# Kernel optimization log

Measured on AMD Instinct MI355X. Metric: run time of the kernel, lower is better.

## Reference

```python
import jax, jax.numpy as jnp
import numpy as np

N = 20000      # nodes
E = 320000     # edges (avg degree 16)
D_IN = 128     # input_dim
HID = 128      # graph_hidden_dim (per-head channels)
HEADS = 4


def setup_inputs() -> dict:
    key = jax.random.key(0)
    ks = jax.random.split(key, 16)
    def gl(k, shape, fan_in):
        return jax.random.normal(k, shape, jnp.float32) / np.float32(np.sqrt(fan_in))
    x = jax.random.normal(ks[0], (N, D_IN), jnp.float32)
    edge_index = jax.random.randint(ks[1], (2, E), 0, N, dtype=jnp.int64)
    # layer 0: in=D_IN, heads=4, concat -> 4*HID
    W0 = gl(ks[2], (D_IN, HEADS * HID), D_IN)
    a_src0 = gl(ks[3], (HEADS, HID), HID)
    a_dst0 = gl(ks[4], (HEADS, HID), HID)
    b0 = jnp.zeros((HEADS * HID,), jnp.float32)
    # layer 1: in=4*HID, heads=4, concat -> 4*HID
    W1 = gl(ks[5], (HEADS * HID, HEADS * HID), HEADS * HID)
    a_src1 = gl(ks[6], (HEADS, HID), HID)
    a_dst1 = gl(ks[7], (HEADS, HID), HID)
    b1 = jnp.zeros((HEADS * HID,), jnp.float32)
    # layer 2: in=4*HID, heads=1, no concat -> HID
    W2 = gl(ks[8], (HEADS * HID, HID), HEADS * HID)
    a_src2 = gl(ks[9], (1, HID), HID)
    a_dst2 = gl(ks[10], (1, HID), HID)
    b2 = jnp.zeros((HID,), jnp.float32)
    # output MLP: HID -> HID//2 -> 1
    Wm1 = gl(ks[11], (HID, HID // 2), HID)
    bm1 = jnp.zeros((HID // 2,), jnp.float32)
    Wm2 = gl(ks[12], (HID // 2, 1), HID // 2)
    bm2 = jnp.zeros((1,), jnp.float32)
    return dict(x=x, edge_index=edge_index, W0=W0, a_src0=a_src0, a_dst0=a_dst0, b0=b0,
                W1=W1, a_src1=a_src1, a_dst1=a_dst1, b1=b1,
                W2=W2, a_src2=a_src2, a_dst2=a_dst2, b2=b2,
                Wm1=Wm1, bm1=bm1, Wm2=Wm2, bm2=bm2)


def _gat(x, src, dst, W, a_s, a_d, b, heads, ch, concat):
    """PyG GATConv: per-head linear, edge attention with LeakyReLU(0.2),
    segment softmax over incoming edges, scatter-add aggregation."""
    n = x.shape[0]
    xl = (x @ W).reshape(n, heads, ch)                      # [N,H,C]
    a_src_n = jnp.einsum('nhc,hc->nh', xl, a_s)             # [N,H]
    a_dst_n = jnp.einsum('nhc,hc->nh', xl, a_d)
    e = jax.nn.leaky_relu(a_src_n[src] + a_dst_n[dst], 0.2) # [E,H]
    m = jax.ops.segment_max(e, dst, num_segments=n)
    ex = jnp.exp(e - m[dst])
    den = jax.ops.segment_sum(ex, dst, num_segments=n)
    alpha = ex / den[dst]                                   # self-loops keep den > 0
    out = jax.ops.segment_sum(alpha[:, :, None] * xl[src], dst, num_segments=n)  # [N,H,C]
    out = out.reshape(n, heads * ch) if concat else out.mean(axis=1)
    return out + b


def reference(x, edge_index, W0, a_src0, a_dst0, b0, W1, a_src1, a_dst1, b1,
              W2, a_src2, a_dst2, b2, Wm1, bm1, Wm2, bm2):
    n = x.shape[0]
    loops = jnp.arange(n, dtype=edge_index.dtype)           # add_self_loops (PyG default)
    src = jnp.concatenate([edge_index[0], loops])
    dst = jnp.concatenate([edge_index[1], loops])
    h = jax.nn.relu(_gat(x, src, dst, W0, a_src0, a_dst0, b0, HEADS, HID, True))
    h = jax.nn.relu(_gat(h, src, dst, W1, a_src1, a_dst1, b1, HEADS, HID, True))
    h = _gat(h, src, dst, W2, a_src2, a_dst2, b2, 1, HID, False)
    g = h.mean(axis=0, keepdims=True)                       # global mean pool, batch=None -> [1,HID]
    g = jax.nn.relu(g @ Wm1 + bm1)
    return g @ Wm2 + bm2                                    # predictions [1,1]
```

## Files before the change

### kernel.cpp

```cpp
#include <hip/hip_runtime.h>
#include <math.h>


#define MAXDEG 96

typedef float f32x4 __attribute__((ext_vector_type(4)));
typedef float f32x2 __attribute__((ext_vector_type(2)));
typedef short s16x8 __attribute__((ext_vector_type(8)));
typedef short s16x4 __attribute__((ext_vector_type(4)));

__device__ inline ushort f2bf(float f) {
  unsigned u = __float_as_uint(f);
  u += 0x7FFF + ((u >> 16) & 1);
  return (ushort)(u >> 16);
}
__device__ inline float bf2f(ushort h) { return __uint_as_float((unsigned)h << 16); }
__device__ inline unsigned char f2fp8(float f) {
  int p = __builtin_amdgcn_cvt_pk_fp8_f32(f, f, 0, false);
  return (unsigned char)(p & 0xFF);
}

__global__ void prep_kernel(
    const float* __restrict__ W0, const float* __restrict__ W1,
    const float* __restrict__ W2, ushort* __restrict__ w0h, ushort* __restrict__ w0l,
    ushort* __restrict__ w1h, ushort* __restrict__ w1l, ushort* __restrict__ w2h,
    ushort* __restrict__ w2l, int* __restrict__ zero_region, int zcount) {
  int idx = blockIdx.x * 256 + threadIdx.x;
  if (idx < zcount) zero_region[idx] = 0;
  const float* W; ushort *th, *tl; int K, N;
  if (idx < 16384)      { W = W0; th = w0h; tl = w0l; K = 128; N = 512; }
  else if (idx < 81920) { idx -= 16384; W = W1; th = w1h; tl = w1l; K = 512; N = 512; }
  else                  { idx -= 81920; W = W2; th = w2h; tl = w2l; K = 512; N = 128; }
  int nn = idx % N;
  int k4 = (idx / N) << 2;
  s16x4 hv, lv;
#pragma unroll
  for (int r = 0; r < 4; ++r) {
    float w = W[(size_t)(k4 + r) * N + nn];
    ushort h = f2bf(w);
    hv[r] = (short)h;
    lv[r] = (short)f2bf(w - bf2f(h));
  }
  *(s16x4*)&th[(size_t)nn * K + k4] = hv;
  *(s16x4*)&tl[(size_t)nn * K + k4] = lv;
}

template <int NC>
__device__ inline void gemm_epilogue(
    f32x4 (&acc)[2][4], unsigned char* __restrict__ Cb, const float* __restrict__ a_s,
    const float* __restrict__ a_d, float* __restrict__ asn, float* __restrict__ adn,
    float (*st_sh)[64][2], int M, int row0, int col0, int hidx,
    int tid, int lane, int wid, int wm, int wn, int fr) {
  constexpr int N = NC * 128;
  float asv[4], adv[4];
#pragma unroll
  for (int j = 0; j < 4; ++j) {
    asv[j] = a_s[hidx * 128 + wn + j * 16 + fr];
    adv[j] = a_d[hidx * 128 + wn + j * 16 + fr];
  }
  int rb = row0 + wm + ((lane >> 4) << 2);
  int cb = col0 + wn + fr;
#pragma unroll
  for (int i = 0; i < 2; ++i)
#pragma unroll
    for (int r = 0; r < 4; ++r) {
      int row = rb + i * 16 + r;
      float sp = 0.f, dp = 0.f;
#pragma unroll
      for (int j = 0; j < 4; ++j) {
        float c = acc[i][j][r];
        sp += c * asv[j];
        dp += c * adv[j];
        if (row < M) Cb[(size_t)row * N + cb + j * 16] = f2fp8(c);
      }
#pragma unroll
      for (int m = 1; m < 16; m <<= 1) {
        sp += __shfl_xor(sp, m);
        dp += __shfl_xor(dp, m);
      }
      if ((lane & 15) == 0) {
        int rowb = wm + i * 16 + ((lane >> 4) << 2) + r;
        st_sh[0][rowb][wid >> 1] = sp;
        st_sh[1][rowb][wid >> 1] = dp;
      }
    }
  __syncthreads();
  if (tid < 64) {
    int row = row0 + tid;
    if (row < M) {
      asn[(size_t)row * NC + hidx] = st_sh[0][tid][0] + st_sh[0][tid][1];
      adn[(size_t)row * NC + hidx] = st_sh[1][tid][0] + st_sh[1][tid][1];
    }
  }
}

template <int NC>
__global__ __launch_bounds__(256, 2) void gemm0_scatter_kernel(
    const float* __restrict__ A, const ushort* __restrict__ Bth,
    const ushort* __restrict__ Btl, unsigned char* __restrict__ Cb,
    const float* __restrict__ a_s, const float* __restrict__ a_d,
    float* __restrict__ asn, float* __restrict__ adn,
    int M, int K,
    const int* __restrict__ ei, int* __restrict__ cursor, int* __restrict__ srcs,
    int E, int n, int scb) {
  __shared__ s16x8 Ash[4][64], Asl[4][64];
  __shared__ s16x8 Bsh[4][128], Bsl[4][128];
  __shared__ float st_sh[2][64][2];

  if ((int)blockIdx.x < scb) {
    int t = blockIdx.x * 256 + threadIdx.x;
    int s, d;
    if (t < E)          { s = ei[t]; d = ei[E + t]; }
    else if (t < E + n) { s = t - E; d = s; }
    else return;
    int pos = atomicAdd(&cursor[d], 1);
    if (pos < MAXDEG) srcs[d * MAXDEG + pos] = s;
    return;
  }

  int id = blockIdx.x - scb;
  int rs = (id / (8 * NC)) * 8 + (id & 7);
  int row0 = rs * 64;
  if (row0 >= M) return;
  int hidx = (id >> 3) % NC;
  int col0 = hidx * 128;
  int tid = threadIdx.x;
  int am = tid >> 2, aq = tid & 3;
  int bn = tid >> 1, bq = (tid & 1) << 1;
  int lane = tid & 63, wid = tid >> 6;
  int wm = (wid & 1) << 5, wn = (wid >> 1) << 6;
  int fr = lane & 15, fqq = lane >> 4;
  f32x4 acc[2][4] = {};
  const float* Arow = A + (size_t)(row0 + am) * K + aq * 8;
  bool avalid = (row0 + am) < M;
  const ushort* bhp = Bth + (size_t)(col0 + bn) * K + bq * 8;
  const ushort* blp = Btl + (size_t)(col0 + bn) * K + bq * 8;

  for (int k0 = 0; k0 < K; k0 += 32) {
    float v[8];
    if (avalid) {
      float4 t0 = *(const float4*)(Arow + k0);
      float4 t1 = *(const float4*)(Arow + k0 + 4);
      v[0] = t0.x; v[1] = t0.y; v[2] = t0.z; v[3] = t0.w;
      v[4] = t1.x; v[5] = t1.y; v[6] = t1.z; v[7] = t1.w;
    } else {
#pragma unroll
      for (int r = 0; r < 8; ++r) v[r] = 0.f;
    }
    s16x8 hv, lv;
#pragma unroll
    for (int r = 0; r < 8; ++r) {
      ushort h = f2bf(v[r]);
      hv[r] = (short)h;
      lv[r] = (short)f2bf(v[r] - bf2f(h));
    }
    Ash[aq][am] = hv;
    Asl[aq][am] = lv;
    Bsh[bq][bn]     = *(const s16x8*)(bhp + k0);
    Bsh[bq + 1][bn] = *(const s16x8*)(bhp + k0 + 8);
    Bsl[bq][bn]     = *(const s16x8*)(blp + k0);
    Bsl[bq + 1][bn] = *(const s16x8*)(blp + k0 + 8);
    __syncthreads();
    s16x8 ah[2], al[2], bh[4], bl[4];
#pragma unroll
    for (int i = 0; i < 2; ++i) {
      ah[i] = Ash[fqq][wm + i * 16 + fr];
      al[i] = Asl[fqq][wm + i * 16 + fr];
    }
#pragma unroll
    for (int j = 0; j < 4; ++j) {
      bh[j] = Bsh[fqq][wn + j * 16 + fr];
      bl[j] = Bsl[fqq][wn + j * 16 + fr];
    }
#pragma unroll
    for (int i = 0; i < 2; ++i)
#pragma unroll
      for (int j = 0; j < 4; ++j) {
        acc[i][j] = __builtin_amdgcn_mfma_f32_16x16x32_bf16(ah[i], bh[j], acc[i][j], 0, 0, 0);
        acc[i][j] = __builtin_amdgcn_mfma_f32_16x16x32_bf16(ah[i], bl[j], acc[i][j], 0, 0, 0);
        acc[i][j] = __builtin_amdgcn_mfma_f32_16x16x32_bf16(al[i], bh[j], acc[i][j], 0, 0, 0);
      }
    __syncthreads();
  }
  gemm_epilogue<NC>(acc, Cb, a_s, a_d, asn, adn, st_sh, M, row0, col0, hidx,
                    tid, lane, wid, wm, wn, fr);
}

template <int NC>
__global__ __launch_bounds__(256, 2) void gemm_bf16a_kernel(
    const ushort* __restrict__ A, const ushort* __restrict__ Bth,
    const ushort* __restrict__ Btl, unsigned char* __restrict__ Cb,
    const float* __restrict__ a_s, const float* __restrict__ a_d,
    float* __restrict__ asn, float* __restrict__ adn,
    int M, int K) {
  __shared__ s16x8 Ash[4][64];
  __shared__ s16x8 Bsh[4][128], Bsl[4][128];
  __shared__ float st_sh[2][64][2];
  int id = blockIdx.x;
  int rs = (id / (8 * NC)) * 8 + (id & 7);
  int row0 = rs * 64;
  if (row0 >= M) return;
  int hidx = (id >> 3) % NC;
  int col0 = hidx * 128;
  int tid = threadIdx.x;
  int am = tid >> 2, aq = tid & 3;
  int bn = tid >> 1, bq = (tid & 1) << 1;
  int lane = tid & 63, wid = tid >> 6;
  int wm = (wid & 1) << 5, wn = (wid >> 1) << 6;
  int fr = lane & 15, fqq = lane >> 4;
  f32x4 acc[2][4] = {};
  const ushort* Arow = A + (size_t)(row0 + am) * K + aq * 8;
  bool avalid = (row0 + am) < M;
  const ushort* bhp = Bth + (size_t)(col0 + bn) * K + bq * 8;
  const ushort* blp = Btl + (size_t)(col0 + bn) * K + bq * 8;
  const s16x8 zero8 = {};

  for (int k0 = 0; k0 < K; k0 += 32) {
    Ash[aq][am] = avalid ? *(const s16x8*)(Arow + k0) : zero8;
    Bsh[bq][bn]     = *(const s16x8*)(bhp + k0);
    Bsh[bq + 1][bn] = *(const s16x8*)(bhp + k0 + 8);
    Bsl[bq][bn]     = *(const s16x8*)(blp + k0);
    Bsl[bq + 1][bn] = *(const s16x8*)(blp + k0 + 8);
    __syncthreads();
    s16x8 ah[2], bh[4], bl[4];
#pragma unroll
    for (int i = 0; i < 2; ++i) ah[i] = Ash[fqq][wm + i * 16 + fr];
#pragma unroll
    for (int j = 0; j < 4; ++j) {
      bh[j] = Bsh[fqq][wn + j * 16 + fr];
      bl[j] = Bsl[fqq][wn + j * 16 + fr];
    }
#pragma unroll
    for (int i = 0; i < 2; ++i)
#pragma unroll
      for (int j = 0; j < 4; ++j) {
        acc[i][j] = __builtin_amdgcn_mfma_f32_16x16x32_bf16(ah[i], bh[j], acc[i][j], 0, 0, 0);
        acc[i][j] = __builtin_amdgcn_mfma_f32_16x16x32_bf16(ah[i], bl[j], acc[i][j], 0, 0, 0);
      }
    __syncthreads();
  }
  gemm_epilogue<NC>(acc, Cb, a_s, a_d, asn, adn, st_sh, M, row0, col0, hidx,
                    tid, lane, wid, wm, wn, fr);
}

template <int NC>
__global__ __launch_bounds__(256, 2) void gemm_bf16a128_kernel(
    const ushort* __restrict__ A, const ushort* __restrict__ Bth,
    const ushort* __restrict__ Btl, unsigned char* __restrict__ Cb,
    const float* __restrict__ a_s, const float* __restrict__ a_d,
    float* __restrict__ asn, float* __restrict__ adn,
    int M, int K) {
  constexpr int N = NC * 128;
  __shared__ s16x8 Ash[4][128];
  __shared__ s16x8 Bsh[4][128], Bsl[4][128];
  __shared__ float st_sh[2][128][2];
  int id = blockIdx.x;
  int rs = (id / (8 * NC)) * 8 + (id & 7);
  int row0 = rs * 128;
  if (row0 >= M) return;
  int hidx = (id >> 3) % NC;
  int col0 = hidx * 128;
  int tid = threadIdx.x;
  int am = tid >> 1, aq = (tid & 1) << 1;
  int bn = tid >> 1, bq = (tid & 1) << 1;
  int lane = tid & 63, wid = tid >> 6;
  int wm = (wid & 1) << 6, wn = (wid >> 1) << 6;
  int fr = lane & 15, fqq = lane >> 4;
  f32x4 acc[4][4] = {};
  const ushort* Arow = A + (size_t)(row0 + am) * K + aq * 8;
  bool avalid = (row0 + am) < M;
  const ushort* bhp = Bth + (size_t)(col0 + bn) * K + bq * 8;
  const ushort* blp = Btl + (size_t)(col0 + bn) * K + bq * 8;
  const s16x8 zero8 = {};

  for (int k0 = 0; k0 < K; k0 += 32) {
    Ash[aq][am]     = avalid ? *(const s16x8*)(Arow + k0) : zero8;
    Ash[aq + 1][am] = avalid ? *(const s16x8*)(Arow + k0 + 8) : zero8;
    Bsh[bq][bn]     = *(const s16x8*)(bhp + k0);
    Bsh[bq + 1][bn] = *(const s16x8*)(bhp + k0 + 8);
    Bsl[bq][bn]     = *(const s16x8*)(blp + k0);
    Bsl[bq + 1][bn] = *(const s16x8*)(blp + k0 + 8);
    __syncthreads();
    s16x8 ah[4], bh[4], bl[4];
#pragma unroll
    for (int i = 0; i < 4; ++i) ah[i] = Ash[fqq][wm + i * 16 + fr];
#pragma unroll
    for (int j = 0; j < 4; ++j) {
      bh[j] = Bsh[fqq][wn + j * 16 + fr];
      bl[j] = Bsl[fqq][wn + j * 16 + fr];
    }
#pragma unroll
    for (int i = 0; i < 4; ++i)
#pragma unroll
      for (int j = 0; j < 4; ++j) {
        acc[i][j] = __builtin_amdgcn_mfma_f32_16x16x32_bf16(ah[i], bh[j], acc[i][j], 0, 0, 0);
        acc[i][j] = __builtin_amdgcn_mfma_f32_16x16x32_bf16(ah[i], bl[j], acc[i][j], 0, 0, 0);
      }
    __syncthreads();
  }
  float asv[4], adv[4];
#pragma unroll
  for (int j = 0; j < 4; ++j) {
    asv[j] = a_s[hidx * 128 + wn + j * 16 + fr];
    adv[j] = a_d[hidx * 128 + wn + j * 16 + fr];
  }
  int rb = row0 + wm + ((lane >> 4) << 2);
  int cb = col0 + wn + fr;
#pragma unroll
  for (int i = 0; i < 4; ++i)
#pragma unroll
    for (int r = 0; r < 4; ++r) {
      int row = rb + i * 16 + r;
      float sp = 0.f, dp = 0.f;
#pragma unroll
      for (int j = 0; j < 4; ++j) {
        float c = acc[i][j][r];
        sp += c * asv[j];
        dp += c * adv[j];
        if (row < M) Cb[(size_t)row * N + cb + j * 16] = f2fp8(c);
      }
#pragma unroll
      for (int m = 1; m < 16; m <<= 1) {
        sp += __shfl_xor(sp, m);
        dp += __shfl_xor(dp, m);
      }
      if ((lane & 15) == 0) {
        int rowb = wm + i * 16 + ((lane >> 4) << 2) + r;
        st_sh[0][rowb][wid >> 1] = sp;
        st_sh[1][rowb][wid >> 1] = dp;
      }
    }
  __syncthreads();
  if (tid < 128) {
    int row = row0 + tid;
    if (row < M) {
      asn[(size_t)row * NC + hidx] = st_sh[0][tid][0] + st_sh[0][tid][1];
      adn[(size_t)row * NC + hidx] = st_sh[1][tid][0] + st_sh[1][tid][1];
    }
  }
}

__global__ __launch_bounds__(256) void agg4_kernel(
    const unsigned char* __restrict__ xl, const float* __restrict__ asn,
    const float* __restrict__ adn, const int* __restrict__ srcs,
    const int* __restrict__ degs, const float* __restrict__ bias,
    ushort* __restrict__ out, int n) {
  __shared__ float alpha_sh[4][4][64];
  __shared__ int src_sh[4][64];
  int wib = threadIdx.x >> 6, lane = threadIdx.x & 63;
  int nd = blockIdx.x * 4 + wib;
  if (nd >= n) return;
  int beg = nd * MAXDEG;
  int deg = min(degs[nd], MAXDEG);
  float4 adl = *(const float4*)&adn[(size_t)nd * 4];
  int ch0 = lane << 3;
  int hm = lane >> 4;
  float den[4] = {0.f, 0.f, 0.f, 0.f};
  float acc[8] = {};

  for (int j0 = 0; j0 < deg; j0 += 64) {
    int j = j0 + lane;
    int s = 0;
    float w0 = 0.f, w1 = 0.f, w2 = 0.f, w3 = 0.f;
    if (j < deg) {
      s = srcs[beg + j];
      float4 av = *(const float4*)&asn[(size_t)s * 4];
      float e;
      e = av.x + adl.x; e = (e > 0.f) ? e : 0.2f * e; w0 = __expf(fminf(e, 30.f));
      e = av.y + adl.y; e = (e > 0.f) ? e : 0.2f * e; w1 = __expf(fminf(e, 30.f));
      e = av.z + adl.z; e = (e > 0.f) ? e : 0.2f * e; w2 = __expf(fminf(e, 30.f));
      e = av.w + adl.w; e = (e > 0.f) ? e : 0.2f * e; w3 = __expf(fminf(e, 30.f));
      den[0] += w0; den[1] += w1; den[2] += w2; den[3] += w3;
    }
    src_sh[wib][lane] = s;
    alpha_sh[wib][0][lane] = w0;
    alpha_sh[wib][1][lane] = w1;
    alpha_sh[wib][2][lane] = w2;
    alpha_sh[wib][3][lane] = w3;
    __builtin_amdgcn_wave_barrier();
    int cl = min(64, deg - j0);
    int jj = 0;
    for (; jj + 8 <= cl; jj += 8) {
      int4 sv0 = *(const int4*)&src_sh[wib][jj];
      int4 sv1 = *(const int4*)&src_sh[wib][jj + 4];
      float4 av0 = *(const float4*)&alpha_sh[wib][hm][jj];
      float4 av1 = *(const float4*)&alpha_sh[wib][hm][jj + 4];
      uint2 v[8];
      v[0] = *(const uint2*)(xl + (size_t)sv0.x * 512 + ch0);
      v[1] = *(const uint2*)(xl + (size_t)sv0.y * 512 + ch0);
      v[2] = *(const uint2*)(xl + (size_t)sv0.z * 512 + ch0);
      v[3] = *(const uint2*)(xl + (size_t)sv0.w * 512 + ch0);
      v[4] = *(const uint2*)(xl + (size_t)sv1.x * 512 + ch0);
      v[5] = *(const uint2*)(xl + (size_t)sv1.y * 512 + ch0);
      v[6] = *(const uint2*)(xl + (size_t)sv1.z * 512 + ch0);
      v[7] = *(const uint2*)(xl + (size_t)sv1.w * 512 + ch0);
      float a[8] = {av0.x, av0.y, av0.z, av0.w, av1.x, av1.y, av1.z, av1.w};
#pragma unroll
      for (int u = 0; u < 8; ++u) {
        f32x2 c01 = __builtin_amdgcn_cvt_pk_f32_fp8((int)v[u].x, false);
        f32x2 c23 = __builtin_amdgcn_cvt_pk_f32_fp8((int)v[u].x, true);
        f32x2 c45 = __builtin_amdgcn_cvt_pk_f32_fp8((int)v[u].y, false);
        f32x2 c67 = __builtin_amdgcn_cvt_pk_f32_fp8((int)v[u].y, true);
        acc[0] += a[u] * c01[0]; acc[1] += a[u] * c01[1];
        acc[2] += a[u] * c23[0]; acc[3] += a[u] * c23[1];
        acc[4] += a[u] * c45[0]; acc[5] += a[u] * c45[1];
        acc[6] += a[u] * c67[0]; acc[7] += a[u] * c67[1];
      }
    }
    for (; jj < cl; ++jj) {
      int s2 = src_sh[wib][jj];
      float a = alpha_sh[wib][hm][jj];
      uint2 v = *(const uint2*)(xl + (size_t)s2 * 512 + ch0);
      f32x2 c01 = __builtin_amdgcn_cvt_pk_f32_fp8((int)v.x, false);
      f32x2 c23 = __builtin_amdgcn_cvt_pk_f32_fp8((int)v.x, true);
      f32x2 c45 = __builtin_amdgcn_cvt_pk_f32_fp8((int)v.y, false);
      f32x2 c67 = __builtin_amdgcn_cvt_pk_f32_fp8((int)v.y, true);
      acc[0] += a * c01[0]; acc[1] += a * c01[1];
      acc[2] += a * c23[0]; acc[3] += a * c23[1];
      acc[4] += a * c45[0]; acc[5] += a * c45[1];
      acc[6] += a * c67[0]; acc[7] += a * c67[1];
    }
    __builtin_amdgcn_wave_barrier();
  }
#pragma unroll
  for (int h = 0; h < 4; ++h)
    for (int m = 1; m < 64; m <<= 1) den[h] += __shfl_xor(den[h], m);
  float d = (hm == 0) ? den[0] : (hm == 1) ? den[1] : (hm == 2) ? den[2] : den[3];
  float inv = 1.f / d;
  s16x8 ob;
#pragma unroll
  for (int i = 0; i < 8; ++i)
    ob[i] = (short)f2bf(fmaxf(acc[i] * inv + bias[ch0 + i], 0.f));
  *(s16x8*)(out + (size_t)nd * 512 + ch0) = ob;
}

__global__ __launch_bounds__(256) void agg1_pool_kernel(
    const unsigned char* __restrict__ xl, const float* __restrict__ asn,
    const float* __restrict__ adn, const int* __restrict__ srcs,
    const int* __restrict__ degs, const float* __restrict__ bias,
    float* __restrict__ g_part, int n) {
  __shared__ float alpha_sh[4][64];
  __shared__ int src_sh[4][64];
  __shared__ float red_sh[4][128];
  int wib = threadIdx.x >> 6, lane = threadIdx.x & 63;
  int nd = blockIdx.x * 4 + wib;
  bool valid = nd < n;
  int ch0 = lane << 1;
  float acc0 = 0.f, acc1 = 0.f;

  if (valid) {
    int beg = nd * MAXDEG;
    int deg = min(degs[nd], MAXDEG);
    float adl = adn[nd];
    float den = 0.f;
    for (int j0 = 0; j0 < deg; j0 += 64) {
      int j = j0 + lane;
      int s = 0;
      float w = 0.f;
      if (j < deg) {
        s = srcs[beg + j];
        float e = asn[s] + adl;
        e = (e > 0.f) ? e : 0.2f * e;
        w = __expf(fminf(e, 30.f));
        den += w;
      }
      src_sh[wib][lane] = s;
      alpha_sh[wib][lane] = w;
      __builtin_amdgcn_wave_barrier();
      int cl = min(64, deg - j0);
      int jj = 0;
      for (; jj + 4 <= cl; jj += 4) {
        int4 sv = *(const int4*)&src_sh[wib][jj];
        float4 av = *(const float4*)&alpha_sh[wib][jj];
        uint v0 = *(const ushort*)(xl + (size_t)sv.x * 128 + ch0);
        uint v1 = *(const ushort*)(xl + (size_t)sv.y * 128 + ch0);
        uint v2 = *(const ushort*)(xl + (size_t)sv.z * 128 + ch0);
        uint v3 = *(const ushort*)(xl + (size_t)sv.w * 128 + ch0);
        f32x2 c0 = __builtin_amdgcn_cvt_pk_f32_fp8((int)v0, false);
        f32x2 c1 = __builtin_amdgcn_cvt_pk_f32_fp8((int)v1, false);
        f32x2 c2 = __builtin_amdgcn_cvt_pk_f32_fp8((int)v2, false);
        f32x2 c3 = __builtin_amdgcn_cvt_pk_f32_fp8((int)v3, false);
        acc0 += av.x * c0[0]; acc1 += av.x * c0[1];
        acc0 += av.y * c1[0]; acc1 += av.y * c1[1];
        acc0 += av.z * c2[0]; acc1 += av.z * c2[1];
        acc0 += av.w * c3[0]; acc1 += av.w * c3[1];
      }
      for (; jj < cl; ++jj) {
        int s2 = src_sh[wib][jj];
        float a = alpha_sh[wib][jj];
        uint v = *(const ushort*)(xl + (size_t)s2 * 128 + ch0);
        f32x2 c = __builtin_amdgcn_cvt_pk_f32_fp8((int)v, false);
        acc0 += a * c[0]; acc1 += a * c[1];
      }
      __builtin_amdgcn_wave_barrier();
    }
    for (int m = 1; m < 64; m <<= 1) den += __shfl_xor(den, m);
    float inv = 1.f / den;
    acc0 = acc0 * inv + bias[ch0 + 0];
    acc1 = acc1 * inv + bias[ch0 + 1];
  }
  red_sh[wib][ch0] = acc0;
  red_sh[wib][ch0 + 1] = acc1;
  __syncthreads();
  if (threadIdx.x < 128) {
    float s = red_sh[0][threadIdx.x] + red_sh[1][threadIdx.x] +
              red_sh[2][threadIdx.x] + red_sh[3][threadIdx.x];
    atomicAdd(&g_part[(blockIdx.x & 63) * 128 + threadIdx.x], s);
  }
}

__global__ void mlp_kernel(const float* __restrict__ g_part,
                           const float* __restrict__ Wm1, const float* __restrict__ bm1,
                           const float* __restrict__ Wm2, const float* __restrict__ bm2,
                           float* __restrict__ out, float invn) {
  __shared__ float gs[128];
  __shared__ float hs[64];
  int t = threadIdx.x;
  float s = 0.f;
  for (int k = 0; k < 64; ++k) s += g_part[k * 128 + t];
  gs[t] = s * invn;
  __syncthreads();
  if (t < 64) {
    float acc = bm1[t];
    for (int c = 0; c < 128; ++c) acc += gs[c] * Wm1[c * 64 + t];
    hs[t] = fmaxf(acc, 0.f);
  }
  __syncthreads();
  if (t == 0) {
    float o = bm2[0];
    for (int j = 0; j < 64; ++j) o += hs[j] * Wm2[j];
    out[0] = o;
  }
}

extern "C" void kernel_launch(void* const* d_in, const int* in_sizes, int n_in,
                              void* d_out, int out_size, void* d_ws, size_t ws_size,
                              hipStream_t stream) {
  const float* x   = (const float*)d_in[0];
  const int*   ei  = (const int*)d_in[1];
  const float* W0  = (const float*)d_in[2];
  const float* as0 = (const float*)d_in[3];
  const float* ad0 = (const float*)d_in[4];
  const float* b0  = (const float*)d_in[5];
  const float* W1  = (const float*)d_in[6];
  const float* as1 = (const float*)d_in[7];
  const float* ad1 = (const float*)d_in[8];
  const float* b1  = (const float*)d_in[9];
  const float* W2  = (const float*)d_in[10];
  const float* as2 = (const float*)d_in[11];
  const float* ad2 = (const float*)d_in[12];
  const float* b2  = (const float*)d_in[13];
  const float* Wm1 = (const float*)d_in[14];
  const float* bm1 = (const float*)d_in[15];
  const float* Wm2 = (const float*)d_in[16];
  const float* bm2 = (const float*)d_in[17];

  const int N = in_sizes[0] / 128;
  const int E = in_sizes[1] / 2;
  const int ET = E + N;

  ushort* hb  = (ushort*)d_ws;
  unsigned char* xlb = (unsigned char*)(hb + (size_t)N * 512);
  float*  asn = (float*)(xlb + (size_t)N * 512);
  float*  adn = asn + (size_t)N * 4;
  float*  gp  = adn + (size_t)N * 4;
  int* cursor = (int*)(gp + 64 * 128);
  int* srcs   = cursor + N;
  ushort* w0h = (ushort*)(((uintptr_t)(srcs + (size_t)N * MAXDEG) + 63) & ~(uintptr_t)63);
  ushort* w0l = w0h + 512 * 128;
  ushort* w1h = w0l + 512 * 128;
  ushort* w1l = w1h + 512 * 512;
  ushort* w2h = w1l + 512 * 512;
  ushort* w2l = w2h + 128 * 512;

  int zcount = 64 * 128 + N;

  prep_kernel<<<384, 256, 0, stream>>>(W0, W1, W2, w0h, w0l, w1h, w1l, w2h, w2l,
                                       gp ? (int*)gp : nullptr, zcount);

  int nwb4 = (N + 3) / 4;
  int rsn = (N + 63) / 64;
  int rsp = ((rsn + 7) / 8) * 8;
  int blk0 = rsp * 4;
  int rs128 = (N + 127) / 128;
  int rsp128 = ((rs128 + 7) / 8) * 8;
  int blk1 = rsp128 * 4;
  int blk2 = rsp;
  int scb  = (ET + 255) / 256;

  gemm0_scatter_kernel<4><<<scb + blk0, 256, 0, stream>>>(
      x, w0h, w0l, xlb, as0, ad0, asn, adn, N, 128,
      ei, cursor, srcs, E, N, scb);
  agg4_kernel<<<nwb4, 256, 0, stream>>>(xlb, asn, adn, srcs, cursor, b0, hb, N);

  gemm_bf16a128_kernel<4><<<blk1, 256, 0, stream>>>(hb, w1h, w1l, xlb, as1, ad1,
                                                    asn, adn, N, 512);
  agg4_kernel<<<nwb4, 256, 0, stream>>>(xlb, asn, adn, srcs, cursor, b1, hb, N);

  gemm_bf16a_kernel<1><<<blk2, 256, 0, stream>>>(hb, w2h, w2l, xlb, as2, ad2,
                                                 asn, adn, N, 512);
  agg1_pool_kernel<<<nwb4, 256, 0, stream>>>(xlb, asn, adn, srcs, cursor, b2, gp, N);

  mlp_kernel<<<1, 128, 0, stream>>>(gp, Wm1, bm1, Wm2, bm2, (float*)d_out,
                                    1.0f / (float)N);
}
```

Measured before the change: 263.4 us.

## Move W1/W2 split into gemm0 launch, reorder blocks, raise gemm1 occupancy

The prep kernel now only splits W0 into bf16 hi/lo parts and zeroes the buffers. The W1/W2 weight splitting moves into the fused gemm0 launch as extra blocks, which now sit after the GEMM blocks together with the edge-scatter blocks, so that work overlaps with the layer-0 GEMM. The layer-1 GEMM's launch bounds are raised from 2 to 3 blocks per CU, which may force register spilling. Block ordering changes which work gets scheduled first.

```diff
diff --git a/kernel.cpp b/kernel.cpp
--- a/kernel.cpp
+++ b/kernel.cpp
@@ -20,17 +20,8 @@
   return (unsigned char)(p & 0xFF);
 }
 
-__global__ void prep_kernel(
-    const float* __restrict__ W0, const float* __restrict__ W1,
-    const float* __restrict__ W2, ushort* __restrict__ w0h, ushort* __restrict__ w0l,
-    ushort* __restrict__ w1h, ushort* __restrict__ w1l, ushort* __restrict__ w2h,
-    ushort* __restrict__ w2l, int* __restrict__ zero_region, int zcount) {
-  int idx = blockIdx.x * 256 + threadIdx.x;
-  if (idx < zcount) zero_region[idx] = 0;
-  const float* W; ushort *th, *tl; int K, N;
-  if (idx < 16384)      { W = W0; th = w0h; tl = w0l; K = 128; N = 512; }
-  else if (idx < 81920) { idx -= 16384; W = W1; th = w1h; tl = w1l; K = 512; N = 512; }
-  else                  { idx -= 81920; W = W2; th = w2h; tl = w2l; K = 512; N = 128; }
+__device__ inline void wsplit_item(const float* __restrict__ W, ushort* __restrict__ th,
+                                   ushort* __restrict__ tl, int K, int N, int idx) {
   int nn = idx % N;
   int k4 = (idx / N) << 2;
   s16x4 hv, lv;
@@ -43,6 +34,14 @@
   }
   *(s16x4*)&th[(size_t)nn * K + k4] = hv;
   *(s16x4*)&tl[(size_t)nn * K + k4] = lv;
+}
+
+__global__ void prep_kernel(const float* __restrict__ W0, ushort* __restrict__ w0h,
+                            ushort* __restrict__ w0l, int* __restrict__ zero_region,
+                            int zcount) {
+  int idx = blockIdx.x * 256 + threadIdx.x;
+  if (idx < zcount) zero_region[idx] = 0;
+  if (idx < 16384) wsplit_item(W0, w0h, w0l, 128, 512, idx);
 }
 
 template <int NC>
@@ -95,20 +94,30 @@
 }
 
 template <int NC>
-__global__ __launch_bounds__(256, 2) void gemm0_scatter_kernel(
+__global__ __launch_bounds__(256, 2) void gemm0_fused_kernel(
     const float* __restrict__ A, const ushort* __restrict__ Bth,
     const ushort* __restrict__ Btl, unsigned char* __restrict__ Cb,
     const float* __restrict__ a_s, const float* __restrict__ a_d,
     float* __restrict__ asn, float* __restrict__ adn,
     int M, int K,
     const int* __restrict__ ei, int* __restrict__ cursor, int* __restrict__ srcs,
-    int E, int n, int scb) {
+    int E, int n, int gemmb, int wsb,
+    const float* __restrict__ W1, const float* __restrict__ W2,
+    ushort* __restrict__ w1h, ushort* __restrict__ w1l,
+    ushort* __restrict__ w2h, ushort* __restrict__ w2l) {
   __shared__ s16x8 Ash[4][64], Asl[4][64];
   __shared__ s16x8 Bsh[4][128], Bsl[4][128];
   __shared__ float st_sh[2][64][2];
 
-  if ((int)blockIdx.x < scb) {
-    int t = blockIdx.x * 256 + threadIdx.x;
+  if ((int)blockIdx.x >= gemmb) {
+    int r = blockIdx.x - gemmb;
+    if (r < wsb) {
+      int idx = r * 256 + threadIdx.x;
+      if (idx < 65536) wsplit_item(W1, w1h, w1l, 512, 512, idx);
+      else             wsplit_item(W2, w2h, w2l, 512, 128, idx - 65536);
+      return;
+    }
+    int t = (r - wsb) * 256 + threadIdx.x;
     int s, d;
     if (t < E)          { s = ei[t]; d = ei[E + t]; }
     else if (t < E + n) { s = t - E; d = s; }
@@ -118,7 +127,7 @@
     return;
   }
 
-  int id = blockIdx.x - scb;
+  int id = blockIdx.x;
   int rs = (id / (8 * NC)) * 8 + (id & 7);
   int row0 = rs * 64;
   if (row0 >= M) return;
@@ -244,7 +253,7 @@
 }
 
 template <int NC>
-__global__ __launch_bounds__(256, 2) void gemm_bf16a128_kernel(
+__global__ __launch_bounds__(256, 3) void gemm_bf16a128_kernel(
     const ushort* __restrict__ A, const ushort* __restrict__ Bth,
     const ushort* __restrict__ Btl, unsigned char* __restrict__ Cb,
     const float* __restrict__ a_s, const float* __restrict__ a_d,
@@ -575,8 +584,8 @@
 
   int zcount = 64 * 128 + N;
 
-  prep_kernel<<<384, 256, 0, stream>>>(W0, W1, W2, w0h, w0l, w1h, w1l, w2h, w2l,
-                                       gp ? (int*)gp : nullptr, zcount);
+  prep_kernel<<<(zcount + 255) / 256, 256, 0, stream>>>(W0, w0h, w0l, (int*)gp,
+                                                        zcount);
 
   int nwb4 = (N + 3) / 4;
   int rsn = (N + 63) / 64;
@@ -586,11 +595,12 @@
   int rsp128 = ((rs128 + 7) / 8) * 8;
   int blk1 = rsp128 * 4;
   int blk2 = rsp;
+  int wsb  = 81920 / 256;
   int scb  = (ET + 255) / 256;
 
-  gemm0_scatter_kernel<4><<<scb + blk0, 256, 0, stream>>>(
+  gemm0_fused_kernel<4><<<blk0 + wsb + scb, 256, 0, stream>>>(
       x, w0h, w0l, xlb, as0, ad0, asn, adn, N, 128,
-      ei, cursor, srcs, E, N, scb);
+      ei, cursor, srcs, E, N, blk0, wsb, W1, W2, w1h, w1l, w2h, w2l);
   agg4_kernel<<<nwb4, 256, 0, stream>>>(xlb, asn, adn, srcs, cursor, b0, hb, N);
 
   gemm_bf16a128_kernel<4><<<blk1, 256, 0, stream>>>(hb, w1h, w1l, xlb, as1, ad1,
```

Result: faster. 253.7 us (-3.7%).
